# Performance work log

Measured on AMD Instinct MI355X. Metric: run time of the kernel, lower is better.

The kernel has to match this reference:

```python
import jax, jax.numpy as jnp
import numpy as np

B, S, D = 2, 2048, 768
H, DK, F = 12, 64, 3072
LN_EPS = 1e-5


def setup_inputs() -> dict:
    key = jax.random.key(0)
    ks = jax.random.split(key, 8)
    w = lambda k, shape: jax.random.normal(k, shape, dtype=jnp.float32) * 0.02
    return {
        "x": jax.random.normal(ks[0], (B, S, D), dtype=jnp.float32),
        "wq_w": w(ks[1], (H, D, DK)), "wq_b": jnp.zeros((H, DK), jnp.float32),
        "wk_w": w(ks[2], (H, D, DK)), "wk_b": jnp.zeros((H, DK), jnp.float32),
        "wv_w": w(ks[3], (H, D, DK)), "wv_b": jnp.zeros((H, DK), jnp.float32),
        "wo_w": w(ks[4], (H * DK, D)), "wo_b": jnp.zeros((D,), jnp.float32),
        "ln_g": jnp.ones((D,), jnp.float32), "ln_b": jnp.zeros((D,), jnp.float32),
        "w1": w(ks[5], (D, F)), "b1": jnp.zeros((F,), jnp.float32),
        "w2": w(ks[6], (F, D)), "b2": jnp.zeros((D,), jnp.float32),
    }


def layer_norm(x, g, b):
    mu = jnp.mean(x, axis=-1, keepdims=True)
    var = jnp.mean(jnp.square(x - mu), axis=-1, keepdims=True)
    return (x - mu) * jax.lax.rsqrt(var + LN_EPS) * g + b


def reference(x, wq_w, wq_b, wk_w, wk_b, wv_w, wv_b, wo_w, wo_b,
              ln_g, ln_b, w1, b1, w2, b2):
    dk = wq_w.shape[-1]
    x_res = x
    h = layer_norm(x, ln_b=ln_b, g=ln_g, b=ln_b) if False else layer_norm(x, ln_g, ln_b)
    # per-head QKV (all heads batched via einsum): [B,H,S,DK]
    q = jnp.einsum("bsd,hdk->bhsk", h, wq_w) + wq_b[None, :, None, :]
    k = jnp.einsum("bsd,hdk->bhsk", h, wk_w) + wk_b[None, :, None, :]
    v = jnp.einsum("bsd,hdk->bhsk", h, wv_w) + wv_b[None, :, None, :]
    scores = jnp.einsum("bhqk,bhsk->bhqs", q, k) / jnp.sqrt(jnp.float32(dk))
    attn = jax.nn.softmax(scores, axis=-1)
    o = jnp.einsum("bhqs,bhsk->bhqk", attn, v)  # [B,H,S,DK]
    Bx, Hx, Sx, Dkx = o.shape
    o = o.transpose(0, 2, 1, 3).reshape(Bx, Sx, Hx * Dkx)  # concat heads
    y = o @ wo_w + wo_b + x_res  # residual 1
    y_res = y
    z = layer_norm(y, ln_g, ln_b)
    z = jax.nn.gelu(z @ w1 + b1, approximate=False) @ w2 + b2
    return z + y_res
```

## Files before the change

kernel.cpp:

```cpp
#include <hip/hip_runtime.h>
#include <hip/hip_bf16.h>
#include <math.h>

typedef __bf16 bf16_t;
typedef __bf16 bf16x8 __attribute__((ext_vector_type(8)));
typedef __bf16 bf16x4 __attribute__((ext_vector_type(4)));
typedef float f32x4 __attribute__((ext_vector_type(4)));

#define MFMA_B16(a, b, c) __builtin_amdgcn_mfma_f32_16x16x32_bf16((a), (b), (c), 0, 0, 0)

static constexpr int Bn = 2, Sn = 2048, Dn = 768, Hn = 12, Fn = 3072;
static constexpr int NTOK = Bn * Sn;
#define QSCALE 0.18033688011112042f

__device__ __forceinline__ void gl_lds16(const bf16_t* g, void* lds) {
  __builtin_amdgcn_global_load_lds(
      (const __attribute__((address_space(1))) uint32_t*)g,
      (__attribute__((address_space(3))) uint32_t*)lds, 16, 0, 0);
}

__global__ __launch_bounds__(256) void k_prep(const float* __restrict__ wq, const float* __restrict__ wk,
                                              const float* __restrict__ wv, const float* __restrict__ wo,
                                              const float* __restrict__ w1, const float* __restrict__ w2,
                                              const float* __restrict__ bq, const float* __restrict__ bk,
                                              const float* __restrict__ bv,
                                              bf16_t* __restrict__ WqkvT, bf16_t* __restrict__ WoT,
                                              bf16_t* __restrict__ W1T, bf16_t* __restrict__ W2T,
                                              float* __restrict__ QKVB,
                                              const float* __restrict__ x, const float* __restrict__ ln_g,
                                              const float* __restrict__ ln_b, bf16_t* __restrict__ Hbuf) {
  int t = blockIdx.x;
  int tid = threadIdx.x;
  if (t >= 1729) {
    int tok = t - 1729;
    const float* xr = x + (size_t)tok * Dn;
    float v0 = xr[tid], v1 = xr[tid + 256], v2 = xr[tid + 512];
    float s = v0 + v1 + v2;
    float ss = v0 * v0 + v1 * v1 + v2 * v2;
    __shared__ float red[8];
#pragma unroll
    for (int off = 32; off > 0; off >>= 1) {
      s += __shfl_down(s, off);
      ss += __shfl_down(ss, off);
    }
    int w = tid >> 6, l = tid & 63;
    if (l == 0) { red[w] = s; red[4 + w] = ss; }
    __syncthreads();
    s = red[0] + red[1] + red[2] + red[3];
    ss = red[4] + red[5] + red[6] + red[7];
    float mu = s * (1.0f / Dn);
    float var = ss * (1.0f / Dn) - mu * mu;
    float rstd = rsqrtf(var + 1e-5f);
    bf16_t* orow = Hbuf + (size_t)tok * Dn;
    orow[tid]       = (bf16_t)((v0 - mu) * rstd * ln_g[tid]       + ln_b[tid]);
    orow[tid + 256] = (bf16_t)((v1 - mu) * rstd * ln_g[tid + 256] + ln_b[tid + 256]);
    orow[tid + 512] = (bf16_t)((v2 - mu) * rstd * ln_g[tid + 512] + ln_b[tid + 512]);
    return;
  }
  if (t == 1728) {
    for (int i = tid; i < 2304; i += 256)
      QKVB[i] = i < 768 ? bq[i] : (i < 1536 ? bk[i - 768] : bv[i - 1536]);
    return;
  }
  __shared__ float T[64][65];
  const float* src;
  bf16_t* dst;
  int P, Q, tp, tq;
  if (t < 432) {
    int pb = t / 12; tp = t - pb * 12; tq = 0;
    int proj = pb / 12, head = pb - proj * 12;
    src = (proj == 0 ? wq : proj == 1 ? wk : wv) + (size_t)head * 768 * 64;
    dst = WqkvT + (size_t)proj * 589824 + (size_t)head * 64 * 768;
    P = 768; Q = 64;
  } else if (t < 576) {
    int u = t - 432; tp = u / 12; tq = u - tp * 12;
    src = wo; dst = WoT; P = 768; Q = 768;
  } else if (t < 1152) {
    int u = t - 576; tp = u / 48; tq = u - tp * 48;
    src = w1; dst = W1T; P = 768; Q = 3072;
  } else {
    int u = t - 1152; tp = u / 12; tq = u - tp * 12;
    src = w2; dst = W2T; P = 3072; Q = 768;
  }
  int j = tid & 63, i0 = tid >> 6;
#pragma unroll
  for (int i = i0; i < 64; i += 4)
    T[i][j] = src[(size_t)(tp * 64 + i) * Q + tq * 64 + j];
  __syncthreads();
#pragma unroll
  for (int i = i0; i < 64; i += 4)
    dst[(size_t)(tq * 64 + i) * P + tp * 64 + j] = (bf16_t)T[j][i];
}

__global__ __launch_bounds__(256) void k_layernorm(const float* __restrict__ x,
                                                   const float* __restrict__ g,
                                                   const float* __restrict__ bb,
                                                   bf16_t* __restrict__ out) {
  int t = blockIdx.x, tid = threadIdx.x;
  const float* xr = x + (size_t)t * Dn;
  float v0 = xr[tid], v1 = xr[tid + 256], v2 = xr[tid + 512];
  float s = v0 + v1 + v2;
  float ss = v0 * v0 + v1 * v1 + v2 * v2;
  __shared__ float red[8];
#pragma unroll
  for (int off = 32; off > 0; off >>= 1) {
    s += __shfl_down(s, off);
    ss += __shfl_down(ss, off);
  }
  int w = tid >> 6, l = tid & 63;
  if (l == 0) { red[w] = s; red[4 + w] = ss; }
  __syncthreads();
  s = red[0] + red[1] + red[2] + red[3];
  ss = red[4] + red[5] + red[6] + red[7];
  float mu = s * (1.0f / Dn);
  float var = ss * (1.0f / Dn) - mu * mu;
  float rstd = rsqrtf(var + 1e-5f);
  bf16_t* orow = out + (size_t)t * Dn;
  orow[tid]       = (bf16_t)((v0 - mu) * rstd * g[tid]       + bb[tid]);
  orow[tid + 256] = (bf16_t)((v1 - mu) * rstd * g[tid + 256] + bb[tid + 256]);
  orow[tid + 512] = (bf16_t)((v2 - mu) * rstd * g[tid + 512] + bb[tid + 512]);
}

enum { EPI_QK = 0, EPI_VT = 1, EPI_Y = 2, EPI_GELU = 3, EPI_OUT = 4 };

template <int MT, int NT, int BK, int EPI, int OCC, int SWZ>
__global__ __launch_bounds__(256, OCC) void k_gemm(const bf16_t* __restrict__ A,
                                                   const bf16_t* __restrict__ Bt,
                                                   int N, int K,
                                                   const float* __restrict__ bias,
                                                   const float* __restrict__ resid,
                                                   void* __restrict__ out0,
                                                   void* __restrict__ out1) {
  constexpr int MI = MT / 32, NI = NT / 32;
  constexpr int WROWS = MT / 2, WCOLS = NT / 2;
  constexpr int KS = BK / 32;
  __shared__ __align__(16) bf16_t As[2][MT * BK];
  __shared__ __align__(16) bf16_t Bs[2][NT * BK];
  const int tid = threadIdx.x;
  const int w = tid >> 6, l = tid & 63;
  const int wm = w >> 1, wn = w & 1;
  const int mloc = l & 15, kblk = l >> 4;
  int bx = blockIdx.x, by = blockIdx.y;
  if constexpr (SWZ) {
    int lin = by * gridDim.x + bx;
    int xcd = lin & 7, s = lin >> 3;
    by = xcd * (gridDim.y >> 3) + s / gridDim.x;
    bx = s - (s / gridDim.x) * gridDim.x;
  }

  f32x4 acc[MI][NI];
#pragma unroll
  for (int i = 0; i < MI; ++i)
#pragma unroll
    for (int j = 0; j < NI; ++j) acc[i][j] = f32x4{0.f, 0.f, 0.f, 0.f};

  const bf16_t* gA = A + (size_t)(by * MT + (tid >> 2)) * K + (tid & 3) * 8;
  const bf16_t* gB = Bt + (size_t)(bx * NT + (tid >> 2)) * K + (tid & 3) * 8;
  const int nk = K / BK;

  auto stage = [&](int kt, int buf) {
#pragma unroll
    for (int h = 0; h < KS; ++h) {
#pragma unroll
      for (int rb = 0; rb < MT / 64; ++rb)
        gl_lds16(gA + (size_t)rb * 64 * K + kt * BK + h * 32,
                 (char*)&As[buf][0] + h * (MT * 64) + rb * 4096 + w * 1024);
#pragma unroll
      for (int rb = 0; rb < NT / 64; ++rb)
        gl_lds16(gB + (size_t)rb * 64 * K + kt * BK + h * 32,
                 (char*)&Bs[buf][0] + h * (NT * 64) + rb * 4096 + w * 1024);
    }
  };

  stage(0, 0);
  for (int kt = 0; kt < nk; ++kt) {
    __syncthreads();
    if (kt + 1 < nk) stage(kt + 1, (kt + 1) & 1);
    const bf16_t* Ab = &As[kt & 1][0];
    const bf16_t* Bb = &Bs[kt & 1][0];
    bf16x8 af[MI][KS], bfv[NI][KS];
#pragma unroll
    for (int mi = 0; mi < MI; ++mi)
#pragma unroll
      for (int ks = 0; ks < KS; ++ks)
        af[mi][ks] = *(const bf16x8*)&Ab[ks * (MT * 32) + (wm * WROWS + mi * 16 + mloc) * 32 + kblk * 8];
#pragma unroll
    for (int ni = 0; ni < NI; ++ni)
#pragma unroll
      for (int ks = 0; ks < KS; ++ks)
        bfv[ni][ks] = *(const bf16x8*)&Bb[ks * (NT * 32) + (wn * WCOLS + ni * 16 + mloc) * 32 + kblk * 8];
#pragma unroll
    for (int ks = 0; ks < KS; ++ks)
#pragma unroll
      for (int mi = 0; mi < MI; ++mi)
#pragma unroll
        for (int ni = 0; ni < NI; ++ni)
          acc[mi][ni] = MFMA_B16(af[mi][ks], bfv[ni][ks], acc[mi][ni]);
  }

  const int gmb = by * MT + wm * WROWS + kblk * 4;
  const int gnb = bx * NT + wn * WCOLS + mloc;
  if constexpr (EPI == EPI_QK) {
    constexpr int TPP = 768 / NT;
    const int proj = bx / TPP;
#pragma unroll
    for (int mi = 0; mi < MI; ++mi)
#pragma unroll
      for (int ni = 0; ni < NI; ++ni) {
        int gn = gnb + ni * 16;
        float bv = bias[gn];
        int gm0 = gmb + mi * 16;
        if (proj == 0) {
          bf16_t* dst = (bf16_t*)out0;
#pragma unroll
          for (int r = 0; r < 4; ++r)
            dst[(size_t)(gm0 + r) * 768 + gn] = (bf16_t)((acc[mi][ni][r] + bv) * QSCALE);
        } else {
          bf16_t* dst = (bf16_t*)out1;
#pragma unroll
          for (int r = 0; r < 4; ++r)
            dst[(size_t)(gm0 + r) * 768 + (gn - 768)] = (bf16_t)(acc[mi][ni][r] + bv);
        }
      }
  } else if constexpr (EPI == EPI_VT) {
    bf16_t* dst = (bf16_t*)out0;
#pragma unroll
    for (int mi = 0; mi < MI; ++mi)
#pragma unroll
      for (int ni = 0; ni < NI; ++ni) {
        int gn = gnb + ni * 16;
        int bq = gn >> 11, sq = gn & 2047;
#pragma unroll
        for (int r = 0; r < 4; ++r) {
          int gm = gmb + mi * 16 + r;
          int hq = gm >> 6, dk = gm & 63;
          dst[((size_t)(bq * Hn + hq) * 64 + dk) * Sn + sq] = (bf16_t)(acc[mi][ni][r] + bias[gm]);
        }
      }
  } else if constexpr (EPI == EPI_GELU) {
    bf16_t* dst = (bf16_t*)out0;
#pragma unroll
    for (int mi = 0; mi < MI; ++mi)
#pragma unroll
      for (int ni = 0; ni < NI; ++ni) {
        int gn = gnb + ni * 16;
        float bv = bias[gn];
#pragma unroll
        for (int r = 0; r < 4; ++r) {
          int gm = gmb + mi * 16 + r;
          float t = acc[mi][ni][r] + bv;
          float ge = 0.5f * t * (1.0f + erff(t * 0.70710678118654752f));
          dst[(size_t)gm * N + gn] = (bf16_t)ge;
        }
      }
  } else {
    float* dst = (float*)out0;
#pragma unroll
    for (int mi = 0; mi < MI; ++mi)
#pragma unroll
      for (int ni = 0; ni < NI; ++ni) {
        int gn = gnb + ni * 16;
        float bv = bias[gn];
#pragma unroll
        for (int r = 0; r < 4; ++r) {
          int gm = gmb + mi * 16 + r;
          dst[(size_t)gm * N + gn] = acc[mi][ni][r] + bv + resid[(size_t)gm * N + gn];
        }
      }
  }
}

__global__ __launch_bounds__(512, 2) void k_attn(const bf16_t* __restrict__ Q,
                                                 const bf16_t* __restrict__ K,
                                                 const bf16_t* __restrict__ VT,
                                                 bf16_t* __restrict__ O) {
  __shared__ __align__(16) bf16_t Ks[2][8192];
  __shared__ __align__(16) bf16_t Vs[2][8192];
  const int tid = threadIdx.x, w = tid >> 6, l = tid & 63;
  const int mloc = l & 15, kblk = l >> 4;
  const int bh = blockIdx.y, b = bh / Hn, h = bh - b * Hn;
  const int q0 = blockIdx.x * 128 + (w >> 2) * 64;
  const int wq = w & 3;

  const size_t qoff = (size_t)(b * Sn + q0 + wq * 16 + mloc) * Dn + h * 64 + kblk * 8;
  const bf16x8 qf0 = *(const bf16x8*)(Q + qoff);
  const bf16x8 qf1 = *(const bf16x8*)(Q + qoff + 32);

  bf16x8 ones;
#pragma unroll
  for (int j = 0; j < 8; ++j) ones[j] = (bf16_t)1.0f;

  const int tq = tid >> 2, q4 = tid & 3;
  const int s0 = (tq & 0x60) | ((tq & 0x0C) << 1) | ((tq & 0x10) >> 2) | (tq & 3);
  const bf16_t* Kg = K + (size_t)(b * Sn + s0) * Dn + h * 64 + q4 * 8;
  const int code0 = 2 * w, code1 = 2 * w + 1;
  const bf16_t* Vg0 = VT + ((size_t)bh * 64 + (code0 & 3) * 16 + (l >> 2)) * Sn + (code0 >> 2) * 32 + (l & 3) * 8;
  const bf16_t* Vg1 = VT + ((size_t)bh * 64 + (code1 & 3) * 16 + (l >> 2)) * Sn + (code1 >> 2) * 32 + (l & 3) * 8;

  f32x4 lacc = f32x4{0.f, 0.f, 0.f, 0.f};
  f32x4 oacc[4];
#pragma unroll
  for (int md = 0; md < 4; ++md) oacc[md] = f32x4{0.f, 0.f, 0.f, 0.f};

  auto stage = [&](int kv0, int buf) {
    gl_lds16(Kg + (size_t)kv0 * Dn,      (char*)&Ks[buf][0] + w * 1024);
    gl_lds16(Kg + (size_t)kv0 * Dn + 32, (char*)&Ks[buf][0] + 8192 + w * 1024);
    gl_lds16(Vg0 + kv0, (char*)&Vs[buf][0] + w * 2048);
    gl_lds16(Vg1 + kv0, (char*)&Vs[buf][0] + w * 2048 + 1024);
  };

  stage(0, 0);
  for (int it = 0; it < Sn / 128; ++it) {
    __syncthreads();
    if (it + 1 < Sn / 128) stage((it + 1) * 128, (it + 1) & 1);
    const bf16_t* Kb = &Ks[it & 1][0];
    const bf16_t* Vb = &Vs[it & 1][0];

    f32x4 st[8];
#pragma unroll
    for (int ns = 0; ns < 8; ++ns) {
      const bf16x8 k0 = *(const bf16x8*)&Kb[(ns * 16 + mloc) * 32 + kblk * 8];
      const bf16x8 k1 = *(const bf16x8*)&Kb[4096 + (ns * 16 + mloc) * 32 + kblk * 8];
      f32x4 a = f32x4{0.f, 0.f, 0.f, 0.f};
      a = MFMA_B16(k0, qf0, a);
      a = MFMA_B16(k1, qf1, a);
      st[ns] = a;
    }

    bf16x8 pb[4];
#pragma unroll
    for (int ns = 0; ns < 8; ++ns)
#pragma unroll
      for (int r = 0; r < 4; ++r)
        pb[ns >> 1][(ns & 1) * 4 + r] = (bf16_t)__builtin_amdgcn_exp2f(st[ns][r]);

#pragma unroll
    for (int c = 0; c < 4; ++c) lacc = MFMA_B16(ones, pb[c], lacc);

#pragma unroll
    for (int md = 0; md < 4; ++md)
#pragma unroll
      for (int c = 0; c < 4; ++c) {
        const bf16x8 v = *(const bf16x8*)&Vb[c * 2048 + (md * 16 + mloc) * 32 + kblk * 8];
        oacc[md] = MFMA_B16(v, pb[c], oacc[md]);
      }
  }

  const float inv = 1.0f / lacc[0];
  const size_t obase = (size_t)(b * Sn + q0 + wq * 16 + mloc) * Dn + h * 64 + kblk * 4;
#pragma unroll
  for (int md = 0; md < 4; ++md) {
    bf16x4 o4;
#pragma unroll
    for (int r = 0; r < 4; ++r) o4[r] = (bf16_t)(oacc[md][r] * inv);
    *(bf16x4*)&O[obase + md * 16] = o4;
  }
}

extern "C" void kernel_launch(void* const* d_in, const int* in_sizes, int n_in,
                              void* d_out, int out_size, void* d_ws, size_t ws_size,
                              hipStream_t stream) {
  (void)in_sizes; (void)n_in; (void)out_size; (void)ws_size;
  const float* x    = (const float*)d_in[0];
  const float* wq_w = (const float*)d_in[1];
  const float* wq_b = (const float*)d_in[2];
  const float* wk_w = (const float*)d_in[3];
  const float* wk_b = (const float*)d_in[4];
  const float* wv_w = (const float*)d_in[5];
  const float* wv_b = (const float*)d_in[6];
  const float* wo_w = (const float*)d_in[7];
  const float* wo_b = (const float*)d_in[8];
  const float* ln_g = (const float*)d_in[9];
  const float* ln_b = (const float*)d_in[10];
  const float* w1   = (const float*)d_in[11];
  const float* b1   = (const float*)d_in[12];
  const float* w2   = (const float*)d_in[13];
  const float* b2   = (const float*)d_in[14];

  char* ws = (char*)d_ws;
  size_t o = 0;
  bf16_t* WqkvT = (bf16_t*)(ws + o); o += (size_t)2304 * 768 * 2;
  bf16_t* WoT   = (bf16_t*)(ws + o); o += (size_t)768 * 768 * 2;
  bf16_t* W1T   = (bf16_t*)(ws + o); o += (size_t)3072 * 768 * 2;
  bf16_t* W2T   = (bf16_t*)(ws + o); o += (size_t)768 * 3072 * 2;
  float*  QKVB  = (float*)(ws + o);  o += (size_t)2304 * 4;
  bf16_t* Hbuf  = (bf16_t*)(ws + o); o += (size_t)NTOK * 768 * 2;
  bf16_t* Qb    = (bf16_t*)(ws + o); o += (size_t)NTOK * 768 * 2;
  bf16_t* Kb    = (bf16_t*)(ws + o); o += (size_t)NTOK * 768 * 2;
  bf16_t* VbT   = (bf16_t*)(ws + o); o += (size_t)NTOK * 768 * 2;
  float*  Ybuf  = (float*)(ws + o);  o += (size_t)NTOK * 768 * 4;
  bf16_t* Zbuf  = (bf16_t*)(ws + o); o += (size_t)NTOK * 768 * 2;
  bf16_t* Ubuf  = (bf16_t*)(ws + o); o += (size_t)NTOK * 3072 * 2;

  k_prep<<<1729 + NTOK, 256, 0, stream>>>(wq_w, wk_w, wv_w, wo_w, w1, w2,
                                          wq_b, wk_b, wv_b, WqkvT, WoT, W1T, W2T, QKVB,
                                          x, ln_g, ln_b, Hbuf);

  k_gemm<128, 64, 64, EPI_QK, 3, 1><<<dim3(24, 32), 256, 0, stream>>>(Hbuf, WqkvT, 1536, 768,
                                                                      QKVB, nullptr, Qb, Kb);

  k_gemm<64, 64, 64, EPI_VT, 4, 0><<<dim3(64, 12), 256, 0, stream>>>(WqkvT + (size_t)2 * 589824, Hbuf,
                                                                     4096, 768, QKVB + 1536, nullptr,
                                                                     VbT, nullptr);

  k_attn<<<dim3(Sn / 128, Bn * Hn), 512, 0, stream>>>(Qb, Kb, VbT, Hbuf);

  k_gemm<64, 64, 64, EPI_Y, 4, 1><<<dim3(12, 64), 256, 0, stream>>>(Hbuf, WoT, 768, 768,
                                                                    wo_b, x, Ybuf, nullptr);

  k_layernorm<<<NTOK, 256, 0, stream>>>(Ybuf, ln_g, ln_b, Zbuf);

  k_gemm<128, 128, 32, EPI_GELU, 3, 1><<<dim3(24, 32), 256, 0, stream>>>(Zbuf, W1T, 3072, 768,
                                                                         b1, nullptr, Ubuf, nullptr);

  k_gemm<64, 64, 64, EPI_OUT, 4, 1><<<dim3(12, 64), 256, 0, stream>>>(Ubuf, W2T, 768, 3072,
                                                                      b2, Ybuf, d_out, nullptr);
}
```

Measured before the change: 271.2 us.

## Give each attention wave two query tiles and retune FFN GEMM K-tiles

```diff
diff --git a/kernel.cpp b/kernel.cpp
--- a/kernel.cpp
+++ b/kernel.cpp
@@ -270,7 +270,7 @@
   }
 }
 
-__global__ __launch_bounds__(512, 2) void k_attn(const bf16_t* __restrict__ Q,
+__global__ __launch_bounds__(256, 2) void k_attn(const bf16_t* __restrict__ Q,
                                                  const bf16_t* __restrict__ K,
                                                  const bf16_t* __restrict__ VT,
                                                  bf16_t* __restrict__ O) {
@@ -279,34 +279,43 @@
   const int tid = threadIdx.x, w = tid >> 6, l = tid & 63;
   const int mloc = l & 15, kblk = l >> 4;
   const int bh = blockIdx.y, b = bh / Hn, h = bh - b * Hn;
-  const int q0 = blockIdx.x * 128 + (w >> 2) * 64;
-  const int wq = w & 3;
-
-  const size_t qoff = (size_t)(b * Sn + q0 + wq * 16 + mloc) * Dn + h * 64 + kblk * 8;
-  const bf16x8 qf0 = *(const bf16x8*)(Q + qoff);
-  const bf16x8 qf1 = *(const bf16x8*)(Q + qoff + 32);
+  const int q0 = blockIdx.x * 128;
+
+  const size_t qoffA = (size_t)(b * Sn + q0 + w * 32 + mloc) * Dn + h * 64 + kblk * 8;
+  const bf16x8 qfa0 = *(const bf16x8*)(Q + qoffA);
+  const bf16x8 qfa1 = *(const bf16x8*)(Q + qoffA + 32);
+  const bf16x8 qfb0 = *(const bf16x8*)(Q + qoffA + (size_t)16 * Dn);
+  const bf16x8 qfb1 = *(const bf16x8*)(Q + qoffA + (size_t)16 * Dn + 32);
 
   bf16x8 ones;
 #pragma unroll
   for (int j = 0; j < 8; ++j) ones[j] = (bf16_t)1.0f;
 
   const int tq = tid >> 2, q4 = tid & 3;
-  const int s0 = (tq & 0x60) | ((tq & 0x0C) << 1) | ((tq & 0x10) >> 2) | (tq & 3);
+  const int s0 = (tq & 0x20) | ((tq & 0x0C) << 1) | ((tq & 0x10) >> 2) | (tq & 3);
   const bf16_t* Kg = K + (size_t)(b * Sn + s0) * Dn + h * 64 + q4 * 8;
-  const int code0 = 2 * w, code1 = 2 * w + 1;
-  const bf16_t* Vg0 = VT + ((size_t)bh * 64 + (code0 & 3) * 16 + (l >> 2)) * Sn + (code0 >> 2) * 32 + (l & 3) * 8;
-  const bf16_t* Vg1 = VT + ((size_t)bh * 64 + (code1 & 3) * 16 + (l >> 2)) * Sn + (code1 >> 2) * 32 + (l & 3) * 8;
-
-  f32x4 lacc = f32x4{0.f, 0.f, 0.f, 0.f};
-  f32x4 oacc[4];
-#pragma unroll
-  for (int md = 0; md < 4; ++md) oacc[md] = f32x4{0.f, 0.f, 0.f, 0.f};
+  const bf16_t* Vg = VT + ((size_t)bh * 64 + (l >> 2)) * Sn + w * 32 + (l & 3) * 8;
+
+  f32x4 lacca = f32x4{0.f, 0.f, 0.f, 0.f};
+  f32x4 laccb = f32x4{0.f, 0.f, 0.f, 0.f};
+  f32x4 oacca[4], oaccb[4];
+#pragma unroll
+  for (int md = 0; md < 4; ++md) {
+    oacca[md] = f32x4{0.f, 0.f, 0.f, 0.f};
+    oaccb[md] = f32x4{0.f, 0.f, 0.f, 0.f};
+  }
 
   auto stage = [&](int kv0, int buf) {
-    gl_lds16(Kg + (size_t)kv0 * Dn,      (char*)&Ks[buf][0] + w * 1024);
-    gl_lds16(Kg + (size_t)kv0 * Dn + 32, (char*)&Ks[buf][0] + 8192 + w * 1024);
-    gl_lds16(Vg0 + kv0, (char*)&Vs[buf][0] + w * 2048);
-    gl_lds16(Vg1 + kv0, (char*)&Vs[buf][0] + w * 2048 + 1024);
+#pragma unroll
+    for (int rb = 0; rb < 2; ++rb)
+#pragma unroll
+      for (int hh = 0; hh < 2; ++hh)
+        gl_lds16(Kg + (size_t)(kv0 + rb * 64) * Dn + hh * 32,
+                 (char*)&Ks[buf][0] + hh * 8192 + rb * 4096 + w * 1024);
+#pragma unroll
+    for (int j = 0; j < 4; ++j)
+      gl_lds16(Vg + kv0 + (size_t)j * 16 * Sn,
+               (char*)&Vs[buf][0] + w * 4096 + j * 1024);
   };
 
   stage(0, 0);
@@ -316,44 +325,60 @@
     const bf16_t* Kb = &Ks[it & 1][0];
     const bf16_t* Vb = &Vs[it & 1][0];
 
-    f32x4 st[8];
+    f32x4 sa[8], sb[8];
 #pragma unroll
     for (int ns = 0; ns < 8; ++ns) {
       const bf16x8 k0 = *(const bf16x8*)&Kb[(ns * 16 + mloc) * 32 + kblk * 8];
       const bf16x8 k1 = *(const bf16x8*)&Kb[4096 + (ns * 16 + mloc) * 32 + kblk * 8];
       f32x4 a = f32x4{0.f, 0.f, 0.f, 0.f};
-      a = MFMA_B16(k0, qf0, a);
-      a = MFMA_B16(k1, qf1, a);
-      st[ns] = a;
+      a = MFMA_B16(k0, qfa0, a);
+      a = MFMA_B16(k1, qfa1, a);
+      sa[ns] = a;
+      f32x4 c = f32x4{0.f, 0.f, 0.f, 0.f};
+      c = MFMA_B16(k0, qfb0, c);
+      c = MFMA_B16(k1, qfb1, c);
+      sb[ns] = c;
     }
 
-    bf16x8 pb[4];
+    bf16x8 pa[4], pbv[4];
 #pragma unroll
     for (int ns = 0; ns < 8; ++ns)
 #pragma unroll
-      for (int r = 0; r < 4; ++r)
-        pb[ns >> 1][(ns & 1) * 4 + r] = (bf16_t)__builtin_amdgcn_exp2f(st[ns][r]);
-
-#pragma unroll
-    for (int c = 0; c < 4; ++c) lacc = MFMA_B16(ones, pb[c], lacc);
+      for (int r = 0; r < 4; ++r) {
+        pa[ns >> 1][(ns & 1) * 4 + r]  = (bf16_t)__builtin_amdgcn_exp2f(sa[ns][r]);
+        pbv[ns >> 1][(ns & 1) * 4 + r] = (bf16_t)__builtin_amdgcn_exp2f(sb[ns][r]);
+      }
+
+#pragma unroll
+    for (int c = 0; c < 4; ++c) {
+      lacca = MFMA_B16(ones, pa[c], lacca);
+      laccb = MFMA_B16(ones, pbv[c], laccb);
+    }
 
 #pragma unroll
     for (int md = 0; md < 4; ++md)
 #pragma unroll
       for (int c = 0; c < 4; ++c) {
         const bf16x8 v = *(const bf16x8*)&Vb[c * 2048 + (md * 16 + mloc) * 32 + kblk * 8];
-        oacc[md] = MFMA_B16(v, pb[c], oacc[md]);
-      }
-  }
-
-  const float inv = 1.0f / lacc[0];
-  const size_t obase = (size_t)(b * Sn + q0 + wq * 16 + mloc) * Dn + h * 64 + kblk * 4;
+        oacca[md] = MFMA_B16(v, pa[c], oacca[md]);
+        oaccb[md] = MFMA_B16(v, pbv[c], oaccb[md]);
+      }
+  }
+
+  const float invA = 1.0f / lacca[0];
+  const float invB = 1.0f / laccb[0];
+  const size_t obA = (size_t)(b * Sn + q0 + w * 32 + mloc) * Dn + h * 64 + kblk * 4;
+  const size_t obB = obA + (size_t)16 * Dn;
 #pragma unroll
   for (int md = 0; md < 4; ++md) {
-    bf16x4 o4;
-#pragma unroll
-    for (int r = 0; r < 4; ++r) o4[r] = (bf16_t)(oacc[md][r] * inv);
-    *(bf16x4*)&O[obase + md * 16] = o4;
+    bf16x4 oa, ob;
+#pragma unroll
+    for (int r = 0; r < 4; ++r) {
+      oa[r] = (bf16_t)(oacca[md][r] * invA);
+      ob[r] = (bf16_t)(oaccb[md][r] * invB);
+    }
+    *(bf16x4*)&O[obA + md * 16] = oa;
+    *(bf16x4*)&O[obB + md * 16] = ob;
   }
 }
 
@@ -403,16 +428,16 @@
                                                                      4096, 768, QKVB + 1536, nullptr,
                                                                      VbT, nullptr);
 
-  k_attn<<<dim3(Sn / 128, Bn * Hn), 512, 0, stream>>>(Qb, Kb, VbT, Hbuf);
+  k_attn<<<dim3(Sn / 128, Bn * Hn), 256, 0, stream>>>(Qb, Kb, VbT, Hbuf);
 
   k_gemm<64, 64, 64, EPI_Y, 4, 1><<<dim3(12, 64), 256, 0, stream>>>(Hbuf, WoT, 768, 768,
                                                                     wo_b, x, Ybuf, nullptr);
 
   k_layernorm<<<NTOK, 256, 0, stream>>>(Ybuf, ln_g, ln_b, Zbuf);
 
-  k_gemm<128, 128, 32, EPI_GELU, 3, 1><<<dim3(24, 32), 256, 0, stream>>>(Zbuf, W1T, 3072, 768,
+  k_gemm<128, 128, 64, EPI_GELU, 2, 1><<<dim3(24, 32), 256, 0, stream>>>(Zbuf, W1T, 3072, 768,
                                                                          b1, nullptr, Ubuf, nullptr);
 
-  k_gemm<64, 64, 64, EPI_OUT, 4, 1><<<dim3(12, 64), 256, 0, stream>>>(Ubuf, W2T, 768, 3072,
-                                                                      b2, Ybuf, d_out, nullptr);
-}
+  k_gemm<64, 64, 128, EPI_OUT, 2, 1><<<dim3(12, 64), 256, 0, stream>>>(Ubuf, W2T, 768, 3072,
+                                                                       b2, Ybuf, d_out, nullptr);
+}
```

Result: slower. 290.7 us (+7.2%).
